# Performance work log

Hardware: AMD Instinct MI355X
Metric: run time of the kernel (lower is better)

Reference implementation:

```python
import jax, jax.numpy as jnp
import numpy as np

N_EMBD = 1024
N_HEAD = 16
D_HEAD = N_EMBD // N_HEAD
B, T = 4, 2048


def _layernorm(x, g, b, eps=1e-5):
    mu = jnp.mean(x, axis=-1, keepdims=True)
    var = jnp.var(x, axis=-1, keepdims=True)
    return (x - mu) * jax.lax.rsqrt(var + eps) * g + b


def setup_inputs() -> dict:
    key = jax.random.key(0)
    ks = jax.random.split(key, 16)
    C = N_EMBD
    s = 0.02
    return {
        "x": jax.random.normal(ks[0], (B, T, C), jnp.float32),
        "ln1_g": jnp.ones((C,), jnp.float32),
        "ln1_b": jnp.zeros((C,), jnp.float32),
        "Wq": jax.random.normal(ks[1], (C, C), jnp.float32) * s,
        "bq": jnp.zeros((C,), jnp.float32),
        "Wk": jax.random.normal(ks[2], (C, C), jnp.float32) * s,
        "bk": jnp.zeros((C,), jnp.float32),
        "Wv": jax.random.normal(ks[3], (C, C), jnp.float32) * s,
        "bv": jnp.zeros((C,), jnp.float32),
        "Wo": jax.random.normal(ks[4], (C, C), jnp.float32) * s,
        "bo": jnp.zeros((C,), jnp.float32),
        "ln2_g": jnp.ones((C,), jnp.float32),
        "ln2_b": jnp.zeros((C,), jnp.float32),
        "W1": jax.random.normal(ks[5], (C, 4 * C), jnp.float32) * s,
        "b1": jnp.zeros((4 * C,), jnp.float32),
        "W2": jax.random.normal(ks[6], (4 * C, C), jnp.float32) * s,
        "b2": jnp.zeros((C,), jnp.float32),
    }


def reference(x, ln1_g, ln1_b, Wq, bq, Wk, bk, Wv, bv, Wo, bo,
              ln2_g, ln2_b, W1, b1, W2, b2):
    Bx, Tx, C = x.shape
    H, D = N_HEAD, D_HEAD

    # --- attention (pre-LN) ---
    h = _layernorm(x, ln1_g, ln1_b)
    q = (h @ Wq + bq).reshape(Bx, Tx, H, D)
    k = (h @ Wk + bk).reshape(Bx, Tx, H, D)
    v = (h @ Wv + bv).reshape(Bx, Tx, H, D)
    att = jnp.einsum("bqhd,bkhd->bhqk", q, k) * (1.0 / jnp.sqrt(jnp.float32(D)))
    causal = jnp.tril(jnp.ones((Tx, Tx), bool))
    att = jnp.where(causal, att, -jnp.inf)
    att = jax.nn.softmax(att, axis=-1)
    y = jnp.einsum("bhqk,bkhd->bqhd", att, v).reshape(Bx, Tx, C)
    x = x + (y @ Wo + bo)

    # --- MLP (pre-LN), exact GELU as in torch F.gelu default ---
    h2 = _layernorm(x, ln2_g, ln2_b)
    m = jax.nn.gelu(h2 @ W1 + b1, approximate=False)
    x = x + (m @ W2 + b2)
    return x
```

## Files before the change

kernel.cpp:

```cpp
#include <hip/hip_runtime.h>
#include <hip/hip_bf16.h>
#include <math.h>

#define C_EMBD 1024
#define T_SEQ  2048
#define BATCH  4
#define NHEAD  16
#define DHEAD  64

typedef __attribute__((ext_vector_type(8))) short bf16x8;
typedef __attribute__((ext_vector_type(4))) float floatx4;

static __device__ __forceinline__ floatx4 mfma16(bf16x8 a, bf16x8 b, floatx4 c) {
    return __builtin_amdgcn_mfma_f32_16x16x32_bf16(a, b, c, 0, 0, 0);
}

static __device__ __forceinline__ void gl2lds16(const void* g, void* l) {
    __builtin_amdgcn_global_load_lds(
        (const __attribute__((address_space(1))) void*)g,
        (__attribute__((address_space(3))) void*)l, 16, 0, 0);
}

__global__ __launch_bounds__(256) void transpose_cvt(
        const float* __restrict__ W, __hip_bfloat16* __restrict__ Wt, int K, int N) {
    __shared__ float tile[32][33];
    const int tid = threadIdx.x;
    const int n0 = blockIdx.x * 32, k0 = blockIdx.y * 32;
    const int r = tid >> 3, c4 = (tid & 7) * 4;
    float4 v = *(const float4*)&W[(size_t)(k0 + r) * N + n0 + c4];
    tile[r][c4 + 0] = v.x; tile[r][c4 + 1] = v.y;
    tile[r][c4 + 2] = v.z; tile[r][c4 + 3] = v.w;
    __syncthreads();
    __align__(8) __hip_bfloat16 ob[4];
    ob[0] = __float2bfloat16(tile[c4 + 0][r]);
    ob[1] = __float2bfloat16(tile[c4 + 1][r]);
    ob[2] = __float2bfloat16(tile[c4 + 2][r]);
    ob[3] = __float2bfloat16(tile[c4 + 3][r]);
    *(short4*)&Wt[(size_t)(n0 + r) * K + k0 + c4] = *(short4*)ob;
}

__global__ __launch_bounds__(256) void ln_bf16(
        const float* __restrict__ x, const float* __restrict__ g,
        const float* __restrict__ b, __hip_bfloat16* __restrict__ out) {
    const int row = blockIdx.x, tid = threadIdx.x;
    const float4 v = ((const float4*)(x + (size_t)row * C_EMBD))[tid];
    float s  = v.x + v.y + v.z + v.w;
    float sq = v.x * v.x + v.y * v.y + v.z * v.z + v.w * v.w;
    #pragma unroll
    for (int off = 1; off < 64; off <<= 1) {
        s  += __shfl_xor(s, off);
        sq += __shfl_xor(sq, off);
    }
    __shared__ float ps[4], pq[4];
    if ((tid & 63) == 0) { ps[tid >> 6] = s; pq[tid >> 6] = sq; }
    __syncthreads();
    s  = ps[0] + ps[1] + ps[2] + ps[3];
    sq = pq[0] + pq[1] + pq[2] + pq[3];
    const float mu   = s * (1.0f / C_EMBD);
    const float var  = sq * (1.0f / C_EMBD) - mu * mu;
    const float rstd = rsqrtf(var + 1e-5f);
    const float4 gv = ((const float4*)g)[tid];
    const float4 bv = ((const float4*)b)[tid];
    __align__(8) __hip_bfloat16 ob[4];
    ob[0] = __float2bfloat16((v.x - mu) * rstd * gv.x + bv.x);
    ob[1] = __float2bfloat16((v.y - mu) * rstd * gv.y + bv.y);
    ob[2] = __float2bfloat16((v.z - mu) * rstd * gv.z + bv.z);
    ob[3] = __float2bfloat16((v.w - mu) * rstd * gv.w + bv.w);
    *(short4*)&out[(size_t)row * C_EMBD + tid * 4] = *(short4*)ob;
}

template <int EP>
__global__ __launch_bounds__(256, 2) void gemm_bt(
        const __hip_bfloat16* __restrict__ A, const __hip_bfloat16* __restrict__ Bt,
        int M, int N, int K,
        const float* __restrict__ ba, const float* __restrict__ bb, const float* __restrict__ bc,
        __hip_bfloat16* __restrict__ o0, __hip_bfloat16* __restrict__ o1,
        __hip_bfloat16* __restrict__ o2, float* __restrict__ of,
        const float* __restrict__ resid) {
    __shared__ __align__(16) __hip_bfloat16 As[128 * 32];
    __shared__ __align__(16) __hip_bfloat16 Bs[128 * 32];
    const int tid  = threadIdx.x;
    const int n0   = blockIdx.x * 128;
    const int m0   = blockIdx.y * 128;
    const int wave = tid >> 6, lane = tid & 63;
    const int l15  = lane & 15, quad = lane >> 4;
    const int wm   = (wave & 1) * 64, wn = (wave >> 1) * 64;
    const int c0   = wave * 2;
    const int sr   = lane >> 2;
    const int sc   = (lane & 3) * 8;

    const floatx4 z4 = {0.f, 0.f, 0.f, 0.f};
    floatx4 acc[4][4];
    #pragma unroll
    for (int i = 0; i < 4; i++)
        #pragma unroll
        for (int j = 0; j < 4; j++) acc[i][j] = z4;

    for (int k0 = 0; k0 < K; k0 += 32) {
        __syncthreads();
        gl2lds16(&A[(m0 + c0 * 16 + sr) * K + k0 + sc],       &As[c0 * 512]);
        gl2lds16(&A[(m0 + (c0 + 1) * 16 + sr) * K + k0 + sc], &As[(c0 + 1) * 512]);
        gl2lds16(&Bt[(n0 + c0 * 16 + sr) * K + k0 + sc],      &Bs[c0 * 512]);
        gl2lds16(&Bt[(n0 + (c0 + 1) * 16 + sr) * K + k0 + sc],&Bs[(c0 + 1) * 512]);
        __syncthreads();
        bf16x8 af[4], bfr[4];
        #pragma unroll
        for (int i = 0; i < 4; i++)
            af[i] = *(const bf16x8*)&As[(wm + i * 16 + l15) * 32 + quad * 8];
        #pragma unroll
        for (int j = 0; j < 4; j++)
            bfr[j] = *(const bf16x8*)&Bs[(wn + j * 16 + l15) * 32 + quad * 8];
        #pragma unroll
        for (int i = 0; i < 4; i++)
            #pragma unroll
            for (int j = 0; j < 4; j++)
                acc[i][j] = mfma16(af[i], bfr[j], acc[i][j]);
    }

    #pragma unroll
    for (int i = 0; i < 4; i++) {
        #pragma unroll
        for (int j = 0; j < 4; j++) {
            const int col = n0 + wn + j * 16 + l15;
            #pragma unroll
            for (int r = 0; r < 4; r++) {
                const int m = m0 + wm + i * 16 + quad * 4 + r;
                float val = acc[i][j][r];
                if (EP == 0) {
                    const int which = col >> 10, cn = col & 1023;
                    const float* bp = (which == 0) ? ba : (which == 1) ? bb : bc;
                    val += bp[cn];
                    const int head = cn >> 6, d = cn & 63;
                    const int bidx = m >> 11, t = m & 2047;
                    if (which == 0) {
                        val *= 0.125f;
                        o0[((bidx * NHEAD + head) * T_SEQ + t) * DHEAD + d] = __float2bfloat16(val);
                    } else if (which == 1) {
                        o1[((bidx * NHEAD + head) * T_SEQ + t) * DHEAD + d] = __float2bfloat16(val);
                    } else {
                        o2[((bidx * NHEAD + head) * DHEAD + d) * T_SEQ + t] = __float2bfloat16(val);
                    }
                } else if (EP == 1) {
                    val += ba[col];
                    of[m * N + col] = resid[m * N + col] + val;
                } else if (EP == 2) {
                    val += ba[col];
                    const float gl = 0.5f * val * (1.0f + erff(val * 0.70710678118654752f));
                    o0[m * N + col] = __float2bfloat16(gl);
                } else {
                    val += ba[col];
                    of[m * N + col] += val;
                }
            }
        }
    }
}

__global__ __launch_bounds__(256, 4) void attn_fa(
        const __hip_bfloat16* __restrict__ q, const __hip_bfloat16* __restrict__ k,
        const __hip_bfloat16* __restrict__ vt, __hip_bfloat16* __restrict__ y) {
    __shared__ __align__(16) __hip_bfloat16 pl[4][32 * 72];
    const int bh = blockIdx.y;
    const int tid = threadIdx.x;
    const int wave = tid >> 6, lane = tid & 63;
    const int l15 = lane & 15, quad = lane >> 4;
    const __hip_bfloat16* qp = q + (size_t)bh * T_SEQ * DHEAD;
    const __hip_bfloat16* kp = k + (size_t)bh * T_SEQ * DHEAD;
    const __hip_bfloat16* vp = vt + (size_t)bh * DHEAD * T_SEQ;
    const int chunk = (wave < 2) ? blockIdx.x : (31 - blockIdx.x);
    const int qw = chunk * 64 + (wave & 1) * 32;

    bf16x8 bq[2][2];
    #pragma unroll
    for (int qi = 0; qi < 2; qi++)
        #pragma unroll
        for (int h = 0; h < 2; h++)
            bq[qi][h] = *(const bf16x8*)&qp[(qw + qi * 16 + l15) * DHEAD + h * 32 + quad * 8];

    const floatx4 z4 = {0.f, 0.f, 0.f, 0.f};
    floatx4 oac[2][4];
    #pragma unroll
    for (int qi = 0; qi < 2; qi++)
        #pragma unroll
        for (int nd = 0; nd < 4; nd++) oac[qi][nd] = z4;
    float li[2] = {0.f, 0.f};

    __hip_bfloat16* myp = &pl[wave][0];

    auto body = [&](int kb, bool diag) {
        bf16x8 kf[4][2];
        #pragma unroll
        for (int nt = 0; nt < 4; nt++)
            #pragma unroll
            for (int h = 0; h < 2; h++)
                kf[nt][h] = *(const bf16x8*)&kp[(kb + nt * 16 + l15) * DHEAD + h * 32 + quad * 8];
        floatx4 sa[2][4];
        #pragma unroll
        for (int qi = 0; qi < 2; qi++)
            #pragma unroll
            for (int nt = 0; nt < 4; nt++) sa[qi][nt] = z4;
        #pragma unroll
        for (int nt = 0; nt < 4; nt++)
            #pragma unroll
            for (int h = 0; h < 2; h++) {
                sa[0][nt] = mfma16(kf[nt][h], bq[0][h], sa[0][nt]);
                sa[1][nt] = mfma16(kf[nt][h], bq[1][h], sa[1][nt]);
            }
        if (diag) {
            #pragma unroll
            for (int qi = 0; qi < 2; qi++)
                #pragma unroll
                for (int nt = 0; nt < 4; nt++)
                    #pragma unroll
                    for (int r = 0; r < 4; r++)
                        if (kb + nt * 16 + quad * 4 + r > qw + qi * 16 + l15)
                            sa[qi][nt][r] = -INFINITY;
        }
        #pragma unroll
        for (int qi = 0; qi < 2; qi++) {
            float sm = 0.f;
            #pragma unroll
            for (int nt = 0; nt < 4; nt++) {
                __align__(8) __hip_bfloat16 pk[4];
                #pragma unroll
                for (int r = 0; r < 4; r++) {
                    const float p = __expf(sa[qi][nt][r]);
                    sm += p;
                    pk[r] = __float2bfloat16(p);
                }
                *(short4*)&myp[(qi * 16 + l15) * 72 + nt * 16 + quad * 4] = *(short4*)pk;
            }
            li[qi] += sm;
        }
        asm volatile("" ::: "memory");
        bf16x8 vf[4][2];
        #pragma unroll
        for (int nd = 0; nd < 4; nd++)
            #pragma unroll
            for (int kh = 0; kh < 2; kh++)
                vf[nd][kh] = *(const bf16x8*)&vp[(nd * 16 + l15) * T_SEQ + kb + kh * 32 + quad * 8];
        asm volatile("s_waitcnt lgkmcnt(0)" ::: "memory");
        bf16x8 pf[2][2];
        #pragma unroll
        for (int qi = 0; qi < 2; qi++)
            #pragma unroll
            for (int kh = 0; kh < 2; kh++)
                pf[qi][kh] = *(const bf16x8*)&myp[(qi * 16 + l15) * 72 + kh * 32 + quad * 8];
        #pragma unroll
        for (int nd = 0; nd < 4; nd++)
            #pragma unroll
            for (int kh = 0; kh < 2; kh++) {
                oac[0][nd] = mfma16(vf[nd][kh], pf[0][kh], oac[0][nd]);
                oac[1][nd] = mfma16(vf[nd][kh], pf[1][kh], oac[1][nd]);
            }
    };

    const int nfull = chunk;
    for (int t = 0; t < nfull; t++) body(t * 64, false);
    body(nfull * 64, true);

    float inv[2];
    #pragma unroll
    for (int qi = 0; qi < 2; qi++) {
        float l = li[qi];
        l += __shfl_xor(l, 16);
        l += __shfl_xor(l, 32);
        inv[qi] = 1.0f / l;
    }
    #pragma unroll
    for (int qi = 0; qi < 2; qi++)
        #pragma unroll
        for (int nd = 0; nd < 4; nd++) {
            __align__(8) __hip_bfloat16 ok[4];
            #pragma unroll
            for (int r = 0; r < 4; r++) ok[r] = __float2bfloat16(oac[qi][nd][r] * inv[qi]);
            *(short4*)&myp[(qi * 16 + l15) * 72 + nd * 16 + quad * 4] = *(short4*)ok;
        }
    asm volatile("s_waitcnt lgkmcnt(0)" ::: "memory");
    const int b = bh >> 4, head = bh & 15;
    #pragma unroll
    for (int half = 0; half < 2; half++) {
        const int row = half * 16 + (lane >> 2);
        const int cb  = (lane & 3) * 16;
        const bf16x8 v0 = *(const bf16x8*)&myp[row * 72 + cb];
        const bf16x8 v1 = *(const bf16x8*)&myp[row * 72 + cb + 8];
        __hip_bfloat16* yr = &y[(size_t)(b * T_SEQ + qw + row) * C_EMBD + head * DHEAD + cb];
        *(bf16x8*)yr       = v0;
        *(bf16x8*)(yr + 8) = v1;
    }
}

extern "C" void kernel_launch(void* const* d_in, const int* in_sizes, int n_in,
                              void* d_out, int out_size, void* d_ws, size_t ws_size,
                              hipStream_t stream) {
    const float* x     = (const float*)d_in[0];
    const float* ln1_g = (const float*)d_in[1];
    const float* ln1_b = (const float*)d_in[2];
    const float* Wq    = (const float*)d_in[3];
    const float* bq    = (const float*)d_in[4];
    const float* Wk    = (const float*)d_in[5];
    const float* bk    = (const float*)d_in[6];
    const float* Wv    = (const float*)d_in[7];
    const float* bv    = (const float*)d_in[8];
    const float* Wo    = (const float*)d_in[9];
    const float* bo    = (const float*)d_in[10];
    const float* ln2_g = (const float*)d_in[11];
    const float* ln2_b = (const float*)d_in[12];
    const float* W1    = (const float*)d_in[13];
    const float* b1    = (const float*)d_in[14];
    const float* W2    = (const float*)d_in[15];
    const float* b2    = (const float*)d_in[16];
    float* out = (float*)d_out;

    char* ws = (char*)d_ws;
    __hip_bfloat16* wqkvt = (__hip_bfloat16*)(ws);
    __hip_bfloat16* wot   = (__hip_bfloat16*)(ws + 6291456);
    __hip_bfloat16* w1t   = (__hip_bfloat16*)(ws + 8388608);
    __hip_bfloat16* w2t   = (__hip_bfloat16*)(ws + 16777216);
    __hip_bfloat16* hbuf  = (__hip_bfloat16*)(ws + 25165824);
    __hip_bfloat16* qbuf  = (__hip_bfloat16*)(ws + 41943040);
    __hip_bfloat16* kbuf  = (__hip_bfloat16*)(ws + 58720256);
    __hip_bfloat16* vbuf  = (__hip_bfloat16*)(ws + 75497472);
    __hip_bfloat16* ybuf  = (__hip_bfloat16*)(ws + 92274688);
    __hip_bfloat16* mbuf  = (__hip_bfloat16*)(ws + 41943040);

    transpose_cvt<<<dim3(32, 32), 256, 0, stream>>>(Wq, wqkvt, 1024, 1024);
    transpose_cvt<<<dim3(32, 32), 256, 0, stream>>>(Wk, wqkvt + 1024 * 1024, 1024, 1024);
    transpose_cvt<<<dim3(32, 32), 256, 0, stream>>>(Wv, wqkvt + 2048 * 1024, 1024, 1024);
    transpose_cvt<<<dim3(32, 32), 256, 0, stream>>>(Wo, wot, 1024, 1024);
    transpose_cvt<<<dim3(128, 32), 256, 0, stream>>>(W1, w1t, 1024, 4096);
    transpose_cvt<<<dim3(32, 128), 256, 0, stream>>>(W2, w2t, 4096, 1024);

    ln_bf16<<<8192, 256, 0, stream>>>(x, ln1_g, ln1_b, hbuf);

    gemm_bt<0><<<dim3(24, 64), 256, 0, stream>>>(hbuf, wqkvt, 8192, 3072, 1024,
        bq, bk, bv, qbuf, kbuf, vbuf, nullptr, nullptr);

    attn_fa<<<dim3(16, 64), 256, 0, stream>>>(qbuf, kbuf, vbuf, ybuf);

    gemm_bt<1><<<dim3(8, 64), 256, 0, stream>>>(ybuf, wot, 8192, 1024, 1024,
        bo, nullptr, nullptr, nullptr, nullptr, nullptr, out, x);

    ln_bf16<<<8192, 256, 0, stream>>>(out, ln2_g, ln2_b, hbuf);

    gemm_bt<2><<<dim3(32, 64), 256, 0, stream>>>(hbuf, w1t, 8192, 4096, 1024,
        b1, nullptr, nullptr, mbuf, nullptr, nullptr, nullptr, nullptr);

    gemm_bt<3><<<dim3(8, 64), 256, 0, stream>>>(mbuf, w2t, 8192, 1024, 4096,
        b2, nullptr, nullptr, nullptr, nullptr, nullptr, out, nullptr);
}
```

Measured before the change: 610.6 us.

## Stage K/V tiles in shared LDS with double buffering and XCD-aware attention scheduling

Restructures the attention kernel so each block loads K and V tiles once into swizzled, double-buffered LDS using direct global-to-LDS loads, shared by all four waves. Before, each wave read K/V from global on its own. Blocks are remapped into a 1D grid so that heads stay on one XCD, and each block handles two balanced causal query tiles (j and 15-j). The Q scale folds in log2(e) so the softmax can use the hardware exp2. The changes add barriers, lower the occupancy hint to 2, and leave some waves idle on the diagonal tiles.

After: 551.8 us. 1.11x faster.

```diff
diff --git a/kernel.cpp b/kernel.cpp
--- a/kernel.cpp
+++ b/kernel.cpp
@@ -10,6 +10,12 @@
 
 typedef __attribute__((ext_vector_type(8))) short bf16x8;
 typedef __attribute__((ext_vector_type(4))) float floatx4;
+
+#if __has_builtin(__builtin_amdgcn_exp2f)
+#define EXP2F __builtin_amdgcn_exp2f
+#else
+#define EXP2F exp2f
+#endif
 
 static __device__ __forceinline__ floatx4 mfma16(bf16x8 a, bf16x8 b, floatx4 c) {
     return __builtin_amdgcn_mfma_f32_16x16x32_bf16(a, b, c, 0, 0, 0);
@@ -133,7 +139,7 @@
                     const int head = cn >> 6, d = cn & 63;
                     const int bidx = m >> 11, t = m & 2047;
                     if (which == 0) {
-                        val *= 0.125f;
+                        val *= 0.18033688011112042f;
                         o0[((bidx * NHEAD + head) * T_SEQ + t) * DHEAD + d] = __float2bfloat16(val);
                     } else if (which == 1) {
                         o1[((bidx * NHEAD + head) * T_SEQ + t) * DHEAD + d] = __float2bfloat16(val);
@@ -156,138 +162,179 @@
     }
 }
 
-__global__ __launch_bounds__(256, 4) void attn_fa(
+__global__ __launch_bounds__(256, 2) void attn_fa(
         const __hip_bfloat16* __restrict__ q, const __hip_bfloat16* __restrict__ k,
         const __hip_bfloat16* __restrict__ vt, __hip_bfloat16* __restrict__ y) {
+    __shared__ __align__(16) __hip_bfloat16 Ks[2][64 * 64];
+    __shared__ __align__(16) __hip_bfloat16 Vs[2][64 * 64];
     __shared__ __align__(16) __hip_bfloat16 pl[4][32 * 72];
-    const int bh = blockIdx.y;
     const int tid = threadIdx.x;
     const int wave = tid >> 6, lane = tid & 63;
     const int l15 = lane & 15, quad = lane >> 4;
+    const int sw  = l15 & 7;
+    const int lr  = lane >> 3;
+    const int gsw = (lane & 7) ^ lr;
+
+    const int lin  = blockIdx.x;
+    const int xcd  = lin & 7;
+    const int slot = lin >> 3;
+    const int bh   = xcd * 8 + (slot >> 3);
+    const int jA   = slot & 7;
+
     const __hip_bfloat16* qp = q + (size_t)bh * T_SEQ * DHEAD;
     const __hip_bfloat16* kp = k + (size_t)bh * T_SEQ * DHEAD;
     const __hip_bfloat16* vp = vt + (size_t)bh * DHEAD * T_SEQ;
-    const int chunk = (wave < 2) ? blockIdx.x : (31 - blockIdx.x);
-    const int qw = chunk * 64 + (wave & 1) * 32;
-
-    bf16x8 bq[2][2];
-    #pragma unroll
-    for (int qi = 0; qi < 2; qi++)
-        #pragma unroll
-        for (int h = 0; h < 2; h++)
-            bq[qi][h] = *(const bf16x8*)&qp[(qw + qi * 16 + l15) * DHEAD + h * 32 + quad * 8];
-
+    __hip_bfloat16* myp = &pl[wave][0];
+    const int b = bh >> 4, head = bh & 15;
     const floatx4 z4 = {0.f, 0.f, 0.f, 0.f};
-    floatx4 oac[2][4];
-    #pragma unroll
-    for (int qi = 0; qi < 2; qi++)
-        #pragma unroll
-        for (int nd = 0; nd < 4; nd++) oac[qi][nd] = z4;
-    float li[2] = {0.f, 0.f};
-
-    __hip_bfloat16* myp = &pl[wave][0];
-
-    auto body = [&](int kb, bool diag) {
-        bf16x8 kf[4][2];
-        #pragma unroll
-        for (int nt = 0; nt < 4; nt++)
+
+    auto stage = [&](const int buf, const int kb) {
+        #pragma unroll
+        for (int j = 0; j < 2; j++) {
+            const int rb = wave * 16 + j * 8;
+            gl2lds16(&kp[(size_t)(kb + rb + lr) * DHEAD + gsw * 8], &Ks[buf][rb * 64]);
+            gl2lds16(&vp[(size_t)(rb + lr) * T_SEQ + kb + gsw * 8], &Vs[buf][rb * 64]);
+        }
+    };
+
+    auto segment = [&](const int tile) {
+        const int q0 = tile * 128;
+        const int qw = q0 + wave * 32;
+        const int cc = tile * 2 + 1;
+
+        bf16x8 bq[2][2];
+        #pragma unroll
+        for (int qi = 0; qi < 2; qi++)
             #pragma unroll
             for (int h = 0; h < 2; h++)
-                kf[nt][h] = *(const bf16x8*)&kp[(kb + nt * 16 + l15) * DHEAD + h * 32 + quad * 8];
-        floatx4 sa[2][4];
+                bq[qi][h] = *(const bf16x8*)&qp[(qw + qi * 16 + l15) * DHEAD + h * 32 + quad * 8];
+
+        floatx4 oac[2][4];
         #pragma unroll
         for (int qi = 0; qi < 2; qi++)
             #pragma unroll
-            for (int nt = 0; nt < 4; nt++) sa[qi][nt] = z4;
-        #pragma unroll
-        for (int nt = 0; nt < 4; nt++)
-            #pragma unroll
-            for (int h = 0; h < 2; h++) {
-                sa[0][nt] = mfma16(kf[nt][h], bq[0][h], sa[0][nt]);
-                sa[1][nt] = mfma16(kf[nt][h], bq[1][h], sa[1][nt]);
+            for (int nd = 0; nd < 4; nd++) oac[qi][nd] = z4;
+        float li[2] = {0.f, 0.f};
+
+        stage(0, 0);
+
+        for (int t = 0; t <= cc; t++) {
+            const int cur = t & 1;
+            if (t < cc) {
+                stage(cur ^ 1, (t + 1) * 64);
+                asm volatile("s_waitcnt vmcnt(4)" ::: "memory");
+            } else {
+                asm volatile("s_waitcnt vmcnt(0)" ::: "memory");
             }
-        if (diag) {
-            #pragma unroll
-            for (int qi = 0; qi < 2; qi++)
+            __builtin_amdgcn_s_barrier();
+            asm volatile("" ::: "memory");
+
+            const int kb = t * 64;
+            const bool act = (kb <= qw + 31);
+            if (act) {
+                const bool dg = (kb + 63 > qw);
+                bf16x8 kf[4][2];
                 #pragma unroll
                 for (int nt = 0; nt < 4; nt++)
                     #pragma unroll
-                    for (int r = 0; r < 4; r++)
-                        if (kb + nt * 16 + quad * 4 + r > qw + qi * 16 + l15)
-                            sa[qi][nt][r] = -INFINITY;
-        }
+                    for (int h = 0; h < 2; h++)
+                        kf[nt][h] = *(const bf16x8*)&Ks[cur][(nt * 16 + l15) * 64 + (((h * 4 + quad) ^ sw) * 8)];
+                floatx4 sa[2][4];
+                #pragma unroll
+                for (int qi = 0; qi < 2; qi++)
+                    #pragma unroll
+                    for (int nt = 0; nt < 4; nt++) sa[qi][nt] = z4;
+                #pragma unroll
+                for (int nt = 0; nt < 4; nt++)
+                    #pragma unroll
+                    for (int h = 0; h < 2; h++) {
+                        sa[0][nt] = mfma16(kf[nt][h], bq[0][h], sa[0][nt]);
+                        sa[1][nt] = mfma16(kf[nt][h], bq[1][h], sa[1][nt]);
+                    }
+                if (dg) {
+                    #pragma unroll
+                    for (int qi = 0; qi < 2; qi++)
+                        #pragma unroll
+                        for (int nt = 0; nt < 4; nt++)
+                            #pragma unroll
+                            for (int r = 0; r < 4; r++)
+                                if (kb + nt * 16 + quad * 4 + r > qw + qi * 16 + l15)
+                                    sa[qi][nt][r] = -INFINITY;
+                }
+                #pragma unroll
+                for (int qi = 0; qi < 2; qi++) {
+                    float sm = 0.f;
+                    #pragma unroll
+                    for (int nt = 0; nt < 4; nt++) {
+                        __align__(8) __hip_bfloat16 pk[4];
+                        #pragma unroll
+                        for (int r = 0; r < 4; r++) {
+                            const float p = EXP2F(sa[qi][nt][r]);
+                            sm += p;
+                            pk[r] = __float2bfloat16(p);
+                        }
+                        *(short4*)&myp[(qi * 16 + l15) * 72 + nt * 16 + quad * 4] = *(short4*)pk;
+                    }
+                    li[qi] += sm;
+                }
+                bf16x8 vf[4][2];
+                #pragma unroll
+                for (int nd = 0; nd < 4; nd++)
+                    #pragma unroll
+                    for (int kh = 0; kh < 2; kh++)
+                        vf[nd][kh] = *(const bf16x8*)&Vs[cur][(nd * 16 + l15) * 64 + (((kh * 4 + quad) ^ sw) * 8)];
+                asm volatile("s_waitcnt lgkmcnt(0)" ::: "memory");
+                bf16x8 pf[2][2];
+                #pragma unroll
+                for (int qi = 0; qi < 2; qi++)
+                    #pragma unroll
+                    for (int kh = 0; kh < 2; kh++)
+                        pf[qi][kh] = *(const bf16x8*)&myp[(qi * 16 + l15) * 72 + kh * 32 + quad * 8];
+                #pragma unroll
+                for (int nd = 0; nd < 4; nd++)
+                    #pragma unroll
+                    for (int kh = 0; kh < 2; kh++) {
+                        oac[0][nd] = mfma16(vf[nd][kh], pf[0][kh], oac[0][nd]);
+                        oac[1][nd] = mfma16(vf[nd][kh], pf[1][kh], oac[1][nd]);
+                    }
+            }
+            asm volatile("" ::: "memory");
+            __builtin_amdgcn_s_barrier();
+        }
+
+        float inv[2];
         #pragma unroll
         for (int qi = 0; qi < 2; qi++) {
-            float sm = 0.f;
-            #pragma unroll
-            for (int nt = 0; nt < 4; nt++) {
-                __align__(8) __hip_bfloat16 pk[4];
-                #pragma unroll
-                for (int r = 0; r < 4; r++) {
-                    const float p = __expf(sa[qi][nt][r]);
-                    sm += p;
-                    pk[r] = __float2bfloat16(p);
-                }
-                *(short4*)&myp[(qi * 16 + l15) * 72 + nt * 16 + quad * 4] = *(short4*)pk;
+            float l = li[qi];
+            l += __shfl_xor(l, 16);
+            l += __shfl_xor(l, 32);
+            inv[qi] = 1.0f / l;
+        }
+        #pragma unroll
+        for (int qi = 0; qi < 2; qi++)
+            #pragma unroll
+            for (int nd = 0; nd < 4; nd++) {
+                __align__(8) __hip_bfloat16 ok[4];
+                #pragma unroll
+                for (int r = 0; r < 4; r++) ok[r] = __float2bfloat16(oac[qi][nd][r] * inv[qi]);
+                *(short4*)&myp[(qi * 16 + l15) * 72 + nd * 16 + quad * 4] = *(short4*)ok;
             }
-            li[qi] += sm;
-        }
-        asm volatile("" ::: "memory");
-        bf16x8 vf[4][2];
-        #pragma unroll
-        for (int nd = 0; nd < 4; nd++)
-            #pragma unroll
-            for (int kh = 0; kh < 2; kh++)
-                vf[nd][kh] = *(const bf16x8*)&vp[(nd * 16 + l15) * T_SEQ + kb + kh * 32 + quad * 8];
         asm volatile("s_waitcnt lgkmcnt(0)" ::: "memory");
-        bf16x8 pf[2][2];
-        #pragma unroll
-        for (int qi = 0; qi < 2; qi++)
-            #pragma unroll
-            for (int kh = 0; kh < 2; kh++)
-                pf[qi][kh] = *(const bf16x8*)&myp[(qi * 16 + l15) * 72 + kh * 32 + quad * 8];
-        #pragma unroll
-        for (int nd = 0; nd < 4; nd++)
-            #pragma unroll
-            for (int kh = 0; kh < 2; kh++) {
-                oac[0][nd] = mfma16(vf[nd][kh], pf[0][kh], oac[0][nd]);
-                oac[1][nd] = mfma16(vf[nd][kh], pf[1][kh], oac[1][nd]);
-            }
+        #pragma unroll
+        for (int half = 0; half < 2; half++) {
+            const int row = half * 16 + (lane >> 2);
+            const int cb  = (lane & 3) * 16;
+            const bf16x8 v0 = *(const bf16x8*)&myp[row * 72 + cb];
+            const bf16x8 v1 = *(const bf16x8*)&myp[row * 72 + cb + 8];
+            __hip_bfloat16* yr = &y[(size_t)(b * T_SEQ + qw + row) * C_EMBD + head * DHEAD + cb];
+            *(bf16x8*)yr       = v0;
+            *(bf16x8*)(yr + 8) = v1;
+        }
+        asm volatile("s_waitcnt vmcnt(0)" ::: "memory");
     };
 
-    const int nfull = chunk;
-    for (int t = 0; t < nfull; t++) body(t * 64, false);
-    body(nfull * 64, true);
-
-    float inv[2];
-    #pragma unroll
-    for (int qi = 0; qi < 2; qi++) {
-        float l = li[qi];
-        l += __shfl_xor(l, 16);
-        l += __shfl_xor(l, 32);
-        inv[qi] = 1.0f / l;
-    }
-    #pragma unroll
-    for (int qi = 0; qi < 2; qi++)
-        #pragma unroll
-        for (int nd = 0; nd < 4; nd++) {
-            __align__(8) __hip_bfloat16 ok[4];
-            #pragma unroll
-            for (int r = 0; r < 4; r++) ok[r] = __float2bfloat16(oac[qi][nd][r] * inv[qi]);
-            *(short4*)&myp[(qi * 16 + l15) * 72 + nd * 16 + quad * 4] = *(short4*)ok;
-        }
-    asm volatile("s_waitcnt lgkmcnt(0)" ::: "memory");
-    const int b = bh >> 4, head = bh & 15;
-    #pragma unroll
-    for (int half = 0; half < 2; half++) {
-        const int row = half * 16 + (lane >> 2);
-        const int cb  = (lane & 3) * 16;
-        const bf16x8 v0 = *(const bf16x8*)&myp[row * 72 + cb];
-        const bf16x8 v1 = *(const bf16x8*)&myp[row * 72 + cb + 8];
-        __hip_bfloat16* yr = &y[(size_t)(b * T_SEQ + qw + row) * C_EMBD + head * DHEAD + cb];
-        *(bf16x8*)yr       = v0;
-        *(bf16x8*)(yr + 8) = v1;
-    }
+    segment(jA);
+    segment(15 - jA);
 }
 
 extern "C" void kernel_launch(void* const* d_in, const int* in_sizes, int n_in,
@@ -336,7 +383,7 @@
     gemm_bt<0><<<dim3(24, 64), 256, 0, stream>>>(hbuf, wqkvt, 8192, 3072, 1024,
         bq, bk, bv, qbuf, kbuf, vbuf, nullptr, nullptr);
 
-    attn_fa<<<dim3(16, 64), 256, 0, stream>>>(qbuf, kbuf, vbuf, ybuf);
+    attn_fa<<<dim3(512), 256, 0, stream>>>(qbuf, kbuf, vbuf, ybuf);
 
     gemm_bt<1><<<dim3(8, 64), 256, 0, stream>>>(ybuf, wot, 8192, 1024, 1024,
         bo, nullptr, nullptr, nullptr, nullptr, nullptr, out, x);
```
